# Performance work log

Measured on AMD Instinct MI355X. Metric: run time of the kernel, lower is better.

## Reference

```python
import jax, jax.numpy as jnp
import numpy as np

C = 128
NUM_GROUPS = 32  # min(32, 128 // 4)
EPS = 1e-6


def group_norm(x, gamma, beta):
    N, Cc, H, W = x.shape
    xg = x.reshape(N, NUM_GROUPS, -1)
    mean = xg.mean(axis=-1, keepdims=True)
    var = ((xg - mean) ** 2).mean(axis=-1, keepdims=True)
    xn = ((xg - mean) * jax.lax.rsqrt(var + EPS)).reshape(N, Cc, H, W)
    return xn * gamma[None, :, None, None] + beta[None, :, None, None]


def conv1x1(x, w, b):
    # w: [C_out, C_in], b: [C_out]; 1x1 conv == channel matmul
    return jnp.einsum('nchw,oc->nohw', x, w) + b[None, :, None, None]


def setup_inputs() -> dict:
    key = jax.random.key(0)
    ks = jax.random.split(key, 11)
    s = 1.0 / np.sqrt(C)
    return {
        'x': jax.random.normal(ks[0], (4, C, 64, 64), dtype=jnp.float32),
        'gamma': jnp.ones((C,), jnp.float32),
        'beta': jnp.zeros((C,), jnp.float32),
        'wq': jax.random.normal(ks[1], (C, C), jnp.float32) * s,
        'bq': jnp.zeros((C,), jnp.float32),
        'wk': jax.random.normal(ks[2], (C, C), jnp.float32) * s,
        'bk': jnp.zeros((C,), jnp.float32),
        'wv': jax.random.normal(ks[3], (C, C), jnp.float32) * s,
        'bv': jnp.zeros((C,), jnp.float32),
        'wo': jax.random.normal(ks[4], (C, C), jnp.float32) * s,
        'bo': jnp.zeros((C,), jnp.float32),
    }


def reference(x, gamma, beta, wq, bq, wk, bk, wv, bv, wo, bo):
    N, Cc, H, W = x.shape
    L = H * W
    xn = group_norm(x, gamma, beta)
    q = conv1x1(xn, wq, bq).reshape(N, Cc, L)  # [N,C,L]
    k = conv1x1(xn, wk, bk).reshape(N, Cc, L)
    v = conv1x1(xn, wv, bv).reshape(N, Cc, L)
    scale = 1.0 / jnp.sqrt(jnp.asarray(Cc, x.dtype))
    scores = jnp.einsum('ncl,ncm->nlm', q, k) * scale  # [N,L,L]
    weights = jax.nn.softmax(scores, axis=-1)
    attn = jnp.einsum('nlm,ncm->ncl', weights, v).reshape(N, Cc, H, W)
    return x + conv1x1(attn, wo, bo)
```

## Files before the change

### kernel.cpp

```cpp
#include <hip/hip_runtime.h>
#include <hip/hip_bf16.h>


#define N_B 4
#define C_D 128
#define L_D 4096
#define SPLIT 4
#define KVB 64
#define FSTEPS ((L_D/SPLIT)/KVB)
#define QSCALE (0.08838834764831845f * 1.4426950408889634f)
#define FIXM 16.0f

using f32x4  = __attribute__((ext_vector_type(4))) float;
using f32x16 = __attribute__((ext_vector_type(16))) float;
using bf16x8 = __attribute__((ext_vector_type(8))) short;

static __device__ __forceinline__ unsigned short f2bf(float f){
  return (unsigned short)((__builtin_bit_cast(unsigned int, f) + 0x8000u) >> 16);
}
static __device__ __forceinline__ float bf2f(unsigned short u){
  unsigned int x = ((unsigned int)u) << 16;
  return __builtin_bit_cast(float, x);
}
static __device__ __forceinline__ unsigned int pk2(float a, float b){
  unsigned int ua = __builtin_bit_cast(unsigned int, a) + 0x8000u;
  unsigned int ub = __builtin_bit_cast(unsigned int, b) + 0x8000u;
  return __builtin_amdgcn_perm(ub, ua, 0x07060302u);
}
static __device__ __forceinline__ float exp2a(float x){
  float r; asm("v_exp_f32 %0, %1" : "=v"(r) : "v"(x)); return r;
}
static __device__ __forceinline__ void gll16(const void* g, void* l){
  __builtin_amdgcn_global_load_lds(
      (const __attribute__((address_space(1))) unsigned int*)g,
      (__attribute__((address_space(3))) unsigned int*)l, 16, 0, 0);
}

__global__ __launch_bounds__(256) void gnw_k(
    const float* __restrict__ x, float* __restrict__ stats,
    const float* __restrict__ wq, const float* __restrict__ wk,
    const float* __restrict__ wv, const float* __restrict__ wo,
    unsigned short* __restrict__ wbf)
{
  int b = blockIdx.x, t = threadIdx.x;
  if (b >= 128){
    int b2 = b - 128;
    int mat = b2 >> 4;
    const float* src = (mat == 0) ? wq : (mat == 1) ? wk : (mat == 2) ? wv : wo;
    int off = (b2 & 15) * 1024 + t * 4;
    float4 v = *(const float4*)(src + off);
    *(uint2*)(wbf + mat*16384 + off) = make_uint2(pk2(v.x, v.y), pk2(v.z, v.w));
    return;
  }
  const float4* p = (const float4*)(x + (size_t)b * (4 * L_D));
  float s = 0.f, ss = 0.f;
#pragma unroll
  for (int i = 0; i < 16; ++i){
    float4 v = p[t + i*256];
    s  += v.x + v.y + v.z + v.w;
    ss += v.x*v.x + v.y*v.y + v.z*v.z + v.w*v.w;
  }
#pragma unroll
  for (int off = 32; off > 0; off >>= 1){
    s  += __shfl_down(s, off);
    ss += __shfl_down(ss, off);
  }
  __shared__ float rs4[4], rss4[4];
  if ((t & 63) == 0){ rs4[t>>6] = s; rss4[t>>6] = ss; }
  __syncthreads();
  if (t == 0){
    s  = rs4[0]+rs4[1]+rs4[2]+rs4[3];
    ss = rss4[0]+rss4[1]+rss4[2]+rss4[3];
    float mean = s * (1.f/16384.f);
    float var  = ss * (1.f/16384.f) - mean*mean;
    if (var < 0.f) var = 0.f;
    stats[2*b]   = mean;
    stats[2*b+1] = rsqrtf(var + 1e-6f);
  }
}

__global__ __launch_bounds__(256) void qkv_k(
    const float* __restrict__ x, const float* __restrict__ stats,
    const float* __restrict__ gamma, const float* __restrict__ beta,
    const unsigned short* __restrict__ wbf,
    const float* __restrict__ bq, const float* __restrict__ bk,
    const float* __restrict__ bv,
    unsigned short* __restrict__ q_ws, unsigned short* __restrict__ k_ws,
    unsigned short* __restrict__ v_ws)
{
  __shared__ unsigned short xnT[64][136];
  __shared__ unsigned short qbuf[64][136];

  int t = threadIdx.x, b = blockIdx.x;
  int wi = b >> 8;
  int bt = b & 255;
  int n = bt >> 6, l0 = (bt & 63) * 64;

  {
    int l = t & 63, cq = t >> 6;
#pragma unroll
    for (int it = 0; it < 8; ++it){
      int c0 = cq*4 + it*16;
      int g  = c0 >> 2;
      float mean = stats[(n*32+g)*2];
      float rstd = stats[(n*32+g)*2+1];
      float vv[4];
#pragma unroll
      for (int jj = 0; jj < 4; ++jj){
        int c = c0 + jj;
        float sc = rstd * gamma[c];
        float bs = beta[c] - mean * sc;
        vv[jj] = x[(size_t)(n*C_D + c)*L_D + l0 + l]*sc + bs;
      }
      *(unsigned int*)&xnT[l][c0]   = pk2(vv[0], vv[1]);
      *(unsigned int*)&xnT[l][c0+2] = pk2(vv[2], vv[3]);
    }
  }
  __syncthreads();

  int w = t >> 6, lane = t & 63, u = lane >> 4, l15 = lane & 15;
  int wc = w >> 1, wl = w & 1;
  const unsigned short* W = wbf + wi*16384;
  const float* Bv = (wi == 0) ? bq : (wi == 1) ? bk : bv;

  f32x4 zz = {0.f,0.f,0.f,0.f};
  f32x4 acc[4][2];
#pragma unroll
  for (int ct = 0; ct < 4; ++ct)
#pragma unroll
    for (int lt = 0; lt < 2; ++lt) acc[ct][lt] = zz;

#pragma unroll
  for (int kst = 0; kst < 4; ++kst){
    bf16x8 bfrag[2];
#pragma unroll
    for (int lt = 0; lt < 2; ++lt)
      bfrag[lt] = *(const bf16x8*)&xnT[32*wl + 16*lt + l15][kst*32 + 8*u];
#pragma unroll
    for (int ct = 0; ct < 4; ++ct){
      bf16x8 af = *(const bf16x8*)(W + (size_t)(64*wc + 16*ct + l15)*C_D + kst*32 + 8*u);
#pragma unroll
      for (int lt = 0; lt < 2; ++lt)
        acc[ct][lt] = __builtin_amdgcn_mfma_f32_16x16x32_bf16(af, bfrag[lt], acc[ct][lt], 0, 0, 0);
    }
  }

  if (wi < 2){
    float qs = (wi == 0) ? QSCALE : 1.0f;
#pragma unroll
    for (int ct = 0; ct < 4; ++ct){
      float bias[4];
#pragma unroll
      for (int r = 0; r < 4; ++r) bias[r] = Bv[64*wc + 16*ct + 4*u + r];
#pragma unroll
      for (int lt = 0; lt < 2; ++lt){
        float v0 = (acc[ct][lt][0] + bias[0]) * qs;
        float v1 = (acc[ct][lt][1] + bias[1]) * qs;
        float v2 = (acc[ct][lt][2] + bias[2]) * qs;
        float v3 = (acc[ct][lt][3] + bias[3]) * qs;
        int row = 32*wl + 16*lt + l15;
        int col = 64*wc + 16*ct + 4*u;
        *(unsigned int*)&qbuf[row][col]   = pk2(v0, v1);
        *(unsigned int*)&qbuf[row][col+2] = pk2(v2, v3);
      }
    }
    __syncthreads();
    {
      int l = t >> 2, ch = t & 3;
      unsigned short* dst = ((wi == 0) ? q_ws : k_ws) + (size_t)(n*L_D + l0 + l)*C_D + ch*32;
#pragma unroll
      for (int i = 0; i < 4; ++i)
        *(uint4*)(dst + i*8) = *(const uint4*)&qbuf[l][ch*32 + i*8];
    }
  } else {
    int p16 = (l15 & 3) | ((l15 & 4) << 1) | ((l15 & 8) >> 1);
#pragma unroll
    for (int ct = 0; ct < 4; ++ct){
      float bias[4];
#pragma unroll
      for (int r = 0; r < 4; ++r) bias[r] = Bv[64*wc + 16*ct + 4*u + r];
#pragma unroll
      for (int lt = 0; lt < 2; ++lt)
#pragma unroll
        for (int r = 0; r < 4; ++r){
          int co = 64*wc + 16*ct + 4*u + r;
          v_ws[(size_t)(n*C_D + co)*L_D + l0 + 32*wl + 16*lt + p16] =
              f2bf(acc[ct][lt][r] + bias[r]);
        }
    }
  }
}

__global__ __launch_bounds__(512, 2) void flash_split_k(
    const unsigned short* __restrict__ q_ws, const unsigned short* __restrict__ k_ws,
    const unsigned short* __restrict__ v_ws,
    unsigned short* __restrict__ po_ws, float* __restrict__ md_ws)
{
  __shared__ __align__(16) char shmem[131072];

  int t = threadIdx.x;
  int phys = blockIdx.x;
  int xcd = phys & 7, j = phys >> 3;
  int pair = xcd*8 + (j & 7);
  int s = j >> 3;
  int n = pair >> 4, lt256 = pair & 15;
  int l0 = lt256 * 256;
  int m_base = s * (L_D / SPLIT);
  int w = t >> 6, lane = t & 63, hi = lane >> 5, l31 = lane & 31;
  int lr = lane >> 4, ls = lane & 15;

  bf16x8 qf[8];
  {
    const unsigned short* qrow = q_ws + ((size_t)(n*L_D + l0 + 32*w + l31))*C_D;
#pragma unroll
    for (int kst = 0; kst < 8; ++kst)
      qf[kst] = *(const bf16x8*)(qrow + 16*kst + 8*hi);
  }

  f32x16 zz16;
#pragma unroll
  for (int i = 0; i < 16; ++i) zz16[i] = 0.f;
  f32x16 accO[4];
#pragma unroll
  for (int ct = 0; ct < 4; ++ct) accO[ct] = zz16;
  float rsum = 0.f;

  const unsigned short* kg[2];
  const unsigned short* vg[2];
  int ldof[2];
#pragma unroll
  for (int i = 0; i < 2; ++i){
    int row = 8*w + 4*i + lr;
    int ub = (ls << 4) ^ ((row & 15) << 4);
    kg[i] = k_ws + ((size_t)(n*L_D + m_base + row))*C_D + (ub >> 1);
    int c    = row + ((ub >> 7) << 6);
    int mloc = (ub & 127) >> 1;
    vg[i] = v_ws + ((size_t)(n*C_D + c))*L_D + m_base + mloc;
    ldof[i] = (8*w + 4*i)*256;
  }

#pragma unroll
  for (int pre = 0; pre < 3; ++pre){
    char* kD = shmem + (pre << 14);
    char* vD = shmem + 65536 + (pre << 14);
    gll16(kg[0] + (size_t)pre*KVB*C_D, kD + ldof[0]);
    gll16(kg[1] + (size_t)pre*KVB*C_D, kD + ldof[1]);
    gll16(vg[0] + pre*KVB, vD + ldof[0]);
    gll16(vg[1] + pre*KVB, vD + ldof[1]);
  }
  asm volatile("s_waitcnt vmcnt(8)" ::: "memory");
  __builtin_amdgcn_s_barrier();
  asm volatile("" ::: "memory");

#pragma unroll 4
  for (int step = 0; step < FSTEPS; ++step){
    int pf = step + 3; if (pf >= FSTEPS) pf = FSTEPS - 1;
    int pb = (step + 3) & 3;
    {
      char* kN = shmem + (pb << 14);
      char* vN = shmem + 65536 + (pb << 14);
      gll16(kg[0] + (size_t)pf*KVB*C_D, kN + ldof[0]);
      gll16(kg[1] + (size_t)pf*KVB*C_D, kN + ldof[1]);
      gll16(vg[0] + pf*KVB, vN + ldof[0]);
      gll16(vg[1] + pf*KVB, vN + ldof[1]);
    }

    char* kB = shmem + ((step & 3) << 14);
    char* vB = shmem + 65536 + ((step & 3) << 14);

    f32x16 accS[2];
#pragma unroll
    for (int mt = 0; mt < 2; ++mt) accS[mt] = zz16;
    __builtin_amdgcn_s_setprio(1);
#pragma unroll
    for (int mt = 0; mt < 2; ++mt){
      int row = 32*mt + l31;
      bf16x8 afr[8];
#pragma unroll
      for (int kst = 0; kst < 8; ++kst)
        afr[kst] = *(const bf16x8*)(kB + row*256 + ((32*kst + 16*hi) ^ ((row & 15) << 4)));
#pragma unroll
      for (int kst = 0; kst < 8; ++kst)
        accS[mt] = __builtin_amdgcn_mfma_f32_32x32x16_bf16(afr[kst], qf[kst], accS[mt], 0, 0, 0);
    }
    __builtin_amdgcn_s_setprio(0);

    union { unsigned int u[8]; bf16x8 h[2]; } Wm[2];
#pragma unroll
    for (int mt = 0; mt < 2; ++mt){
      float p[16];
#pragma unroll
      for (int r = 0; r < 16; ++r) p[r] = exp2a(accS[mt][r] - FIXM);
      float s0 = (p[0]+p[1])+(p[2]+p[3]),   s1 = (p[4]+p[5])+(p[6]+p[7]);
      float s2 = (p[8]+p[9])+(p[10]+p[11]), s3 = (p[12]+p[13])+(p[14]+p[15]);
      rsum += (s0+s1)+(s2+s3);
#pragma unroll
      for (int wd = 0; wd < 8; ++wd) Wm[mt].u[wd] = pk2(p[2*wd], p[2*wd+1]);
    }

    __builtin_amdgcn_s_setprio(1);
#pragma unroll
    for (int sl = 0; sl < 4; ++sl){
      bf16x8 pf2 = Wm[sl >> 1].h[sl & 1];
      bf16x8 vfr[4];
#pragma unroll
      for (int ct = 0; ct < 4; ++ct){
        int c = 32*ct + l31, vrow = c & 63;
        int lb = ((c >> 6) << 7) + 32*sl + 16*hi;
        vfr[ct] = *(const bf16x8*)(vB + vrow*256 + (lb ^ ((vrow & 15) << 4)));
      }
#pragma unroll
      for (int ct = 0; ct < 4; ++ct)
        accO[ct] = __builtin_amdgcn_mfma_f32_32x32x16_bf16(vfr[ct], pf2, accO[ct], 0, 0, 0);
    }
    __builtin_amdgcn_s_setprio(0);

    asm volatile("s_waitcnt vmcnt(8)" ::: "memory");
    __builtin_amdgcn_s_barrier();
    asm volatile("" ::: "memory");
  }

  asm volatile("s_waitcnt vmcnt(0)" ::: "memory");
  __builtin_amdgcn_s_barrier();
  asm volatile("" ::: "memory");

  rsum += __shfl_xor(rsum, 32);

  char* tB = shmem;
  {
    int lloc = 32*w + l31;
    int tsw = (lloc & 15) << 4;
    char* tr = tB + (size_t)lloc*256;
#pragma unroll
    for (int ct = 0; ct < 4; ++ct)
#pragma unroll
      for (int q = 0; q < 4; ++q){
        int cb2 = 64*ct + 16*q + 8*hi;
        *(unsigned int*)(tr + ((cb2    ) ^ tsw)) = pk2(accO[ct][4*q+0], accO[ct][4*q+1]);
        *(unsigned int*)(tr + ((cb2 + 4) ^ tsw)) = pk2(accO[ct][4*q+2], accO[ct][4*q+3]);
      }
  }
  __syncthreads();
  {
    int row2 = t >> 1, hf2 = t & 1;
    int tile = row2 >> 7, lrow = row2 & 127;
    size_t pb = ((size_t)((n*32 + 2*lt256 + tile)*SPLIT + s)) * (size_t)(128*128);
    unsigned short* dst = po_ws + pb + (size_t)lrow*128 + hf2*64;
    const char* srcr = tB + row2*256;
    int sw2 = (row2 & 15) << 4;
#pragma unroll
    for (int i = 0; i < 8; ++i)
      *(uint4*)(dst + 8*i) = *(const uint4*)(srcr + ((hf2*128 + 16*i) ^ sw2));
  }
  if (lane < 32){
    int lg = 32*w + lane;
    int tile2 = lg >> 7, lrow2 = lg & 127;
    size_t mb2 = ((size_t)((n*32 + 2*lt256 + tile2)*SPLIT + s)) * 128;
    md_ws[mb2 + lrow2] = rsum;
  }
}

__global__ __launch_bounds__(256) void combine_k(
    const unsigned short* __restrict__ po_ws, const float* __restrict__ md_ws,
    const float* __restrict__ x, const unsigned short* __restrict__ wo_bf,
    const float* __restrict__ bo, float* __restrict__ out)
{
  __shared__ __align__(16) char aB[16384];

  int t = threadIdx.x, b = blockIdx.x;
  int xcd = b & 7, j = b >> 3;
  int pair = xcd*8 + (j & 7);
  int quarter = j >> 3;
  int n = pair >> 4, lt256 = pair & 15;
  int lt64 = lt256*4 + quarter;
  int f = lt64 >> 1, loff = (lt64 & 1)*64, l0 = lt64*64;
  size_t pbase = ((size_t)((n*32 + f)*SPLIT)) * (size_t)(128*128);
  size_t mbase = ((size_t)((n*32 + f)*SPLIT)) * 128;

  {
    int l = t >> 2, q = t & 3;
    float Dg = 0.f;
#pragma unroll
    for (int s2 = 0; s2 < SPLIT; ++s2)
      Dg += md_ws[mbase + s2*128 + loff + l];
    float inv = 1.0f / Dg;

    float a[32];
#pragma unroll
    for (int i = 0; i < 32; ++i) a[i] = 0.f;
#pragma unroll
    for (int s2 = 0; s2 < SPLIT; ++s2){
      const uint4* p = (const uint4*)(po_ws + pbase + (size_t)s2*(128*128)
                                      + (size_t)(loff + l)*128 + q*32);
#pragma unroll
      for (int i = 0; i < 4; ++i){
        uint4 uv = p[i];
        unsigned int uu[4] = {uv.x, uv.y, uv.z, uv.w};
#pragma unroll
        for (int j2 = 0; j2 < 4; ++j2){
          a[8*i + 2*j2]     += bf2f((unsigned short)(uu[j2] & 0xffffu));
          a[8*i + 2*j2 + 1] += bf2f((unsigned short)(uu[j2] >> 16));
        }
      }
    }
    char* ar = aB + l*256;
    int asw = (l & 7) << 4;
#pragma unroll
    for (int i = 0; i < 16; ++i){
      int cb = q*64 + 4*i;
      *(unsigned int*)(ar + (cb ^ asw)) = pk2(a[2*i]*inv, a[2*i+1]*inv);
    }
  }
  __syncthreads();

  int w = t >> 6, lane = t & 63, hi = lane >> 5, l31 = lane & 31;
  int lh = w >> 1, ch = w & 1;
  f32x16 acc[2];
#pragma unroll
  for (int ci = 0; ci < 2; ++ci)
#pragma unroll
    for (int i = 0; i < 16; ++i) acc[ci][i] = 0.f;

#pragma unroll
  for (int kst = 0; kst < 8; ++kst){
    int row = 32*lh + l31;
    bf16x8 bfg = *(const bf16x8*)(aB + row*256 + ((32*kst + 16*hi) ^ ((row & 7) << 4)));
#pragma unroll
    for (int ci = 0; ci < 2; ++ci){
      bf16x8 af = *(const bf16x8*)(wo_bf + (size_t)(64*ch + 32*ci + l31)*C_D + 16*kst + 8*hi);
      acc[ci] = __builtin_amdgcn_mfma_f32_32x32x16_bf16(af, bfg, acc[ci], 0, 0, 0);
    }
  }
#pragma unroll
  for (int ci = 0; ci < 2; ++ci)
#pragma unroll
    for (int r = 0; r < 16; ++r){
      int o = 64*ch + 32*ci + (r & 3) + 8*(r >> 2) + 4*hi;
      size_t idx = (size_t)(n*C_D + o)*L_D + l0 + 32*lh + l31;
      out[idx] = x[idx] + bo[o] + acc[ci][r];
    }
}

extern "C" void kernel_launch(void* const* d_in, const int* in_sizes, int n_in,
                              void* d_out, int out_size, void* d_ws, size_t ws_size,
                              hipStream_t stream) {
  const float* x     = (const float*)d_in[0];
  const float* gamma = (const float*)d_in[1];
  const float* beta  = (const float*)d_in[2];
  const float* wq    = (const float*)d_in[3];
  const float* bq    = (const float*)d_in[4];
  const float* wk    = (const float*)d_in[5];
  const float* bk    = (const float*)d_in[6];
  const float* wv    = (const float*)d_in[7];
  const float* bv    = (const float*)d_in[8];
  const float* wo    = (const float*)d_in[9];
  const float* bo    = (const float*)d_in[10];
  float* out = (float*)d_out;

  char* ws = (char*)d_ws;
  float* stats          = (float*)ws;
  unsigned short* q_ws  = (unsigned short*)(ws + 4096);
  unsigned short* k_ws  = q_ws + (size_t)N_B * L_D * C_D;
  unsigned short* v_ws  = k_ws + (size_t)N_B * L_D * C_D;
  unsigned short* po_ws = v_ws + (size_t)N_B * L_D * C_D;
  float* md_ws          = (float*)(po_ws + (size_t)N_B * 32 * SPLIT * 128 * 128);
  unsigned short* wbf   = (unsigned short*)(md_ws + (size_t)N_B * 32 * SPLIT * 128);

  gnw_k<<<192, 256, 0, stream>>>(x, stats, wq, wk, wv, wo, wbf);
  qkv_k<<<768, 256, 0, stream>>>(x, stats, gamma, beta, wbf, bq, bk, bv,
                                 q_ws, k_ws, v_ws);
  flash_split_k<<<256, 512, 0, stream>>>(q_ws, k_ws, v_ws, po_ws, md_ws);
  combine_k<<<256, 256, 0, stream>>>(po_ws, md_ws, x, wbf + 3*16384, bo, out);
}
```

Before: 73.52 us.

## Software-pipeline flash loop so QK of next tile overlaps softmax and PV

Restructures the split-K flash attention main loop into a software pipeline. The QK^T scores for the next KV tile are computed while exp2/pack of the previous scores and the PV MFMAs on the previous V tile run interleaved in the same step. The loop is manually unrolled by two with ping-pong score registers. Prefetch distance drops from 3 to 2 tiles to free an LDS buffer for the lagging V tile. This aims to hide transcendental and packing latency behind matrix-core work, at the cost of more live registers and a shallower global prefetch.

```diff
diff --git a/kernel.cpp b/kernel.cpp
--- a/kernel.cpp
+++ b/kernel.cpp
@@ -191,6 +191,105 @@
   }
 }
 
+#define STEPBODY(STEP, SIN0, SIN1, SOUT0, SOUT1, DOQK)                           \
+  {                                                                              \
+    const int step_ = (STEP);                                                    \
+    int pfi = step_ + 2; if (pfi > FSTEPS-1) pfi = FSTEPS-1;                     \
+    int pbb = (step_ + 2) & 3;                                                   \
+    {                                                                            \
+      char* kN = shmem + (pbb << 14);                                            \
+      char* vN = shmem + 65536 + (pbb << 14);                                    \
+      gll16(kg[0] + (size_t)pfi*KVB*C_D, kN + ldof[0]);                          \
+      gll16(kg[1] + (size_t)pfi*KVB*C_D, kN + ldof[1]);                          \
+      gll16(vg[0] + pfi*KVB, vN + ldof[0]);                                      \
+      gll16(vg[1] + pfi*KVB, vN + ldof[1]);                                      \
+    }                                                                            \
+    char* kB = shmem + ((step_ & 3) << 14);                                      \
+    char* vP = shmem + 65536 + (((step_ - 1) & 3) << 14);                        \
+    const bool doQK = (DOQK);                                                    \
+    float p0[16], p1[16];                                                        \
+    union Wu { unsigned int u[8]; bf16x8 h[2]; } Wm0, Wm1;                       \
+    __builtin_amdgcn_s_setprio(1);                                               \
+                                  \
+    if (doQK){                                                                   \
+      bf16x8 afr[8];                                                             \
+      _Pragma("unroll")                                                          \
+      for (int k = 0; k < 8; ++k)                                                \
+        afr[k] = *(const bf16x8*)(kB + l31*256 +                                 \
+                   ((32*k + 16*hi) ^ ((l31 & 15) << 4)));                        \
+      SOUT0 = zz16;                                                              \
+      _Pragma("unroll")                                                          \
+      for (int k = 0; k < 8; ++k){                                               \
+        SOUT0 = __builtin_amdgcn_mfma_f32_32x32x16_bf16(afr[k], qf[k], SOUT0, 0, 0, 0); \
+        p0[2*k]   = exp2a(SIN0[2*k]   - FIXM);                                   \
+        p0[2*k+1] = exp2a(SIN0[2*k+1] - FIXM);                                   \
+      }                                                                          \
+    } else {                                                                     \
+      _Pragma("unroll")                                                          \
+      for (int r = 0; r < 16; ++r) p0[r] = exp2a(SIN0[r] - FIXM);                \
+    }                                                                            \
+                                     \
+    if (doQK){                                                                   \
+      bf16x8 afr[8];                                                             \
+      _Pragma("unroll")                                                          \
+      for (int k = 0; k < 8; ++k)                                                \
+        afr[k] = *(const bf16x8*)(kB + (32 + l31)*256 +                          \
+                   ((32*k + 16*hi) ^ ((l31 & 15) << 4)));                        \
+      SOUT1 = zz16;                                                              \
+      _Pragma("unroll")                                                          \
+      for (int k = 0; k < 8; ++k){                                               \
+        SOUT1 = __builtin_amdgcn_mfma_f32_32x32x16_bf16(afr[k], qf[k], SOUT1, 0, 0, 0); \
+        Wm0.u[k] = pk2(p0[2*k], p0[2*k+1]);                                      \
+      }                                                                          \
+    } else {                                                                     \
+      _Pragma("unroll")                                                          \
+      for (int k = 0; k < 8; ++k) Wm0.u[k] = pk2(p0[2*k], p0[2*k+1]);            \
+    }                                                                            \
+    rsum += (((p0[0]+p0[1])+(p0[2]+p0[3])) + ((p0[4]+p0[5])+(p0[6]+p0[7])))      \
+          + (((p0[8]+p0[9])+(p0[10]+p0[11])) + ((p0[12]+p0[13])+(p0[14]+p0[15])));\
+                                \
+    _Pragma("unroll")                                                            \
+    for (int sl = 0; sl < 2; ++sl){                                              \
+      bf16x8 pfv = Wm0.h[sl];                                                    \
+      bf16x8 vfr[4];                                                             \
+      _Pragma("unroll")                                                          \
+      for (int ct = 0; ct < 4; ++ct){                                            \
+        int c = 32*ct + l31, vrow = c & 63;                                      \
+        int lb = ((c >> 6) << 7) + 32*sl + 16*hi;                                \
+        vfr[ct] = *(const bf16x8*)(vP + vrow*256 + (lb ^ ((vrow & 15) << 4)));   \
+      }                                                                          \
+      _Pragma("unroll")                                                          \
+      for (int ct = 0; ct < 4; ++ct){                                            \
+        accO[ct] = __builtin_amdgcn_mfma_f32_32x32x16_bf16(vfr[ct], pfv, accO[ct], 0, 0, 0); \
+        p1[8*sl + 2*ct]     = exp2a(SIN1[8*sl + 2*ct]     - FIXM);               \
+        p1[8*sl + 2*ct + 1] = exp2a(SIN1[8*sl + 2*ct + 1] - FIXM);               \
+      }                                                                          \
+    }                                                                            \
+    _Pragma("unroll")                                                            \
+    for (int k = 0; k < 8; ++k) Wm1.u[k] = pk2(p1[2*k], p1[2*k+1]);              \
+    rsum += (((p1[0]+p1[1])+(p1[2]+p1[3])) + ((p1[4]+p1[5])+(p1[6]+p1[7])))      \
+          + (((p1[8]+p1[9])+(p1[10]+p1[11])) + ((p1[12]+p1[13])+(p1[14]+p1[15])));\
+                                                            \
+    _Pragma("unroll")                                                            \
+    for (int sl = 2; sl < 4; ++sl){                                              \
+      bf16x8 pfv = Wm1.h[sl & 1];                                                \
+      bf16x8 vfr[4];                                                             \
+      _Pragma("unroll")                                                          \
+      for (int ct = 0; ct < 4; ++ct){                                            \
+        int c = 32*ct + l31, vrow = c & 63;                                      \
+        int lb = ((c >> 6) << 7) + 32*sl + 16*hi;                                \
+        vfr[ct] = *(const bf16x8*)(vP + vrow*256 + (lb ^ ((vrow & 15) << 4)));   \
+      }                                                                          \
+      _Pragma("unroll")                                                          \
+      for (int ct = 0; ct < 4; ++ct)                                             \
+        accO[ct] = __builtin_amdgcn_mfma_f32_32x32x16_bf16(vfr[ct], pfv, accO[ct], 0, 0, 0); \
+    }                                                                            \
+    __builtin_amdgcn_s_setprio(0);                                               \
+    asm volatile("s_waitcnt vmcnt(4)" ::: "memory");                             \
+    __builtin_amdgcn_s_barrier();                                                \
+    asm volatile("" ::: "memory");                                               \
+  }
+
 __global__ __launch_bounds__(512, 2) void flash_split_k(
     const unsigned short* __restrict__ q_ws, const unsigned short* __restrict__ k_ws,
     const unsigned short* __restrict__ v_ws,
@@ -248,76 +347,33 @@
     gll16(vg[0] + pre*KVB, vD + ldof[0]);
     gll16(vg[1] + pre*KVB, vD + ldof[1]);
   }
-  asm volatile("s_waitcnt vmcnt(8)" ::: "memory");
+  asm volatile("s_waitcnt vmcnt(4)" ::: "memory");
   __builtin_amdgcn_s_barrier();
   asm volatile("" ::: "memory");
 
-#pragma unroll 4
-  for (int step = 0; step < FSTEPS; ++step){
-    int pf = step + 3; if (pf >= FSTEPS) pf = FSTEPS - 1;
-    int pb = (step + 3) & 3;
-    {
-      char* kN = shmem + (pb << 14);
-      char* vN = shmem + 65536 + (pb << 14);
-      gll16(kg[0] + (size_t)pf*KVB*C_D, kN + ldof[0]);
-      gll16(kg[1] + (size_t)pf*KVB*C_D, kN + ldof[1]);
-      gll16(vg[0] + pf*KVB, vN + ldof[0]);
-      gll16(vg[1] + pf*KVB, vN + ldof[1]);
-    }
-
-    char* kB = shmem + ((step & 3) << 14);
-    char* vB = shmem + 65536 + ((step & 3) << 14);
-
-    f32x16 accS[2];
-#pragma unroll
-    for (int mt = 0; mt < 2; ++mt) accS[mt] = zz16;
+  f32x16 sA0, sA1, sB0, sB1;
+  {
     __builtin_amdgcn_s_setprio(1);
-#pragma unroll
-    for (int mt = 0; mt < 2; ++mt){
-      int row = 32*mt + l31;
-      bf16x8 afr[8];
-#pragma unroll
-      for (int kst = 0; kst < 8; ++kst)
-        afr[kst] = *(const bf16x8*)(kB + row*256 + ((32*kst + 16*hi) ^ ((row & 15) << 4)));
-#pragma unroll
-      for (int kst = 0; kst < 8; ++kst)
-        accS[mt] = __builtin_amdgcn_mfma_f32_32x32x16_bf16(afr[kst], qf[kst], accS[mt], 0, 0, 0);
-    }
+    sA0 = zz16; sA1 = zz16;
+    bf16x8 afr[8];
+#pragma unroll
+    for (int k = 0; k < 8; ++k)
+      afr[k] = *(const bf16x8*)(shmem + l31*256 + ((32*k + 16*hi) ^ ((l31 & 15) << 4)));
+#pragma unroll
+    for (int k = 0; k < 8; ++k)
+      sA0 = __builtin_amdgcn_mfma_f32_32x32x16_bf16(afr[k], qf[k], sA0, 0, 0, 0);
+#pragma unroll
+    for (int k = 0; k < 8; ++k)
+      afr[k] = *(const bf16x8*)(shmem + (32 + l31)*256 + ((32*k + 16*hi) ^ ((l31 & 15) << 4)));
+#pragma unroll
+    for (int k = 0; k < 8; ++k)
+      sA1 = __builtin_amdgcn_mfma_f32_32x32x16_bf16(afr[k], qf[k], sA1, 0, 0, 0);
     __builtin_amdgcn_s_setprio(0);
-
-    union { unsigned int u[8]; bf16x8 h[2]; } Wm[2];
-#pragma unroll
-    for (int mt = 0; mt < 2; ++mt){
-      float p[16];
-#pragma unroll
-      for (int r = 0; r < 16; ++r) p[r] = exp2a(accS[mt][r] - FIXM);
-      float s0 = (p[0]+p[1])+(p[2]+p[3]),   s1 = (p[4]+p[5])+(p[6]+p[7]);
-      float s2 = (p[8]+p[9])+(p[10]+p[11]), s3 = (p[12]+p[13])+(p[14]+p[15]);
-      rsum += (s0+s1)+(s2+s3);
-#pragma unroll
-      for (int wd = 0; wd < 8; ++wd) Wm[mt].u[wd] = pk2(p[2*wd], p[2*wd+1]);
-    }
-
-    __builtin_amdgcn_s_setprio(1);
-#pragma unroll
-    for (int sl = 0; sl < 4; ++sl){
-      bf16x8 pf2 = Wm[sl >> 1].h[sl & 1];
-      bf16x8 vfr[4];
-#pragma unroll
-      for (int ct = 0; ct < 4; ++ct){
-        int c = 32*ct + l31, vrow = c & 63;
-        int lb = ((c >> 6) << 7) + 32*sl + 16*hi;
-        vfr[ct] = *(const bf16x8*)(vB + vrow*256 + (lb ^ ((vrow & 15) << 4)));
-      }
-#pragma unroll
-      for (int ct = 0; ct < 4; ++ct)
-        accO[ct] = __builtin_amdgcn_mfma_f32_32x32x16_bf16(vfr[ct], pf2, accO[ct], 0, 0, 0);
-    }
-    __builtin_amdgcn_s_setprio(0);
-
-    asm volatile("s_waitcnt vmcnt(8)" ::: "memory");
-    __builtin_amdgcn_s_barrier();
-    asm volatile("" ::: "memory");
+  }
+
+  for (int e = 1; e < 17; e += 2){
+    STEPBODY(e,     sA0, sA1, sB0, sB1, true)
+    STEPBODY(e + 1, sB0, sB1, sA0, sA1, (e + 1 < FSTEPS))
   }
 
   asm volatile("s_waitcnt vmcnt(0)" ::: "memory");
```

New measurement: 73.74 us. About the same (+0.3%).

## Software-pipeline flash loop so QK of next tile overlaps softmax and PV

Applied to the files above, without the earlier changes.

Restructures the split-K flash attention main loop into a software pipeline. Each phase computes QK scores for tile u while exp2 and PV for tile u-1 are interleaved with the MFMAs, using ping-pong score registers. Prefetch depth drops from three tiles ahead to two, and extra barriers split each step into four sub-phases so that waves stay in lockstep. The aim is to hide exp/pack latency behind matrix ops, at the cost of more barriers, higher register pressure and a shallower prefetch.

```diff
diff --git a/kernel.cpp b/kernel.cpp
--- a/kernel.cpp
+++ b/kernel.cpp
@@ -191,6 +191,122 @@
   }
 }
 
+#define BARRIER() do { __builtin_amdgcn_s_barrier(); asm volatile("" ::: "memory"); } while(0)
+
+#define PHASESTEP(U, SIN0, SIN1, SOUT0, SOUT1, DOQK, DOPV)                       \
+  {                                                                              \
+    const int u_ = (U);                                                          \
+    char* kB = shmem + ((u_ & 3) << 14);                                         \
+    char* vP = shmem + 65536 + (((u_ - 1) & 3) << 14);                           \
+    const bool doQK = (DOQK), doPV = (DOPV);                                     \
+    float p0[16], p1[16];                                                        \
+    union Wu { unsigned int u[8]; bf16x8 h[2]; } Wm0, Wm1;                       \
+             \
+    {                                                                            \
+      bf16x8 afr[8];                                                             \
+      if (doQK){                                                                 \
+        _Pragma("unroll")                                                        \
+        for (int k = 0; k < 8; ++k)                                              \
+          afr[k] = *(const bf16x8*)(kB + l31*256 + ((32*k + 16*hi) ^ swz));      \
+      }                                                                          \
+      { int nu = u_ + 2; int nk = nu > FSTEPS-1 ? FSTEPS-1 : nu;                 \
+        char* kN = shmem + ((nu & 3) << 14);                                     \
+        char* vN = shmem + 65536 + ((nu & 3) << 14);                             \
+        gll16(kg[0] + (size_t)nk*KVB*C_D, kN + ldof[0]);                         \
+        gll16(kg[1] + (size_t)nk*KVB*C_D, kN + ldof[1]);                         \
+        gll16(vg[0] + nk*KVB, vN + ldof[0]);                                     \
+        gll16(vg[1] + nk*KVB, vN + ldof[1]); }                                   \
+      BARRIER();                                                                 \
+      __builtin_amdgcn_s_setprio(1);                                             \
+      if (doQK) SOUT0 = zz16;                                                    \
+      _Pragma("unroll")                                                          \
+      for (int k = 0; k < 8; ++k){                                               \
+        if (doQK) SOUT0 = __builtin_amdgcn_mfma_f32_32x32x16_bf16(afr[k], qf[k], SOUT0, 0, 0, 0); \
+        if (doPV){ p0[2*k] = exp2a(SIN0[2*k] - FIXM);                            \
+                   p0[2*k+1] = exp2a(SIN0[2*k+1] - FIXM); }                      \
+      }                                                                          \
+      __builtin_amdgcn_s_setprio(0);                                             \
+      BARRIER();                                                                 \
+    }                                                                            \
+                        \
+    {                                                                            \
+      bf16x8 afr[8];                                                             \
+      if (doQK){                                                                 \
+        _Pragma("unroll")                                                        \
+        for (int k = 0; k < 8; ++k)                                              \
+          afr[k] = *(const bf16x8*)(kB + (32 + l31)*256 + ((32*k + 16*hi) ^ swz)); \
+      }                                                                          \
+      BARRIER();                                                                 \
+      __builtin_amdgcn_s_setprio(1);                                             \
+      if (doQK) SOUT1 = zz16;                                                    \
+      _Pragma("unroll")                                                          \
+      for (int k = 0; k < 8; ++k){                                               \
+        if (doQK) SOUT1 = __builtin_amdgcn_mfma_f32_32x32x16_bf16(afr[k], qf[k], SOUT1, 0, 0, 0); \
+        if (doPV) Wm0.u[k] = pk2(p0[2*k], p0[2*k+1]);                            \
+      }                                                                          \
+      if (doPV)                                                                  \
+        rsum += (((p0[0]+p0[1])+(p0[2]+p0[3])) + ((p0[4]+p0[5])+(p0[6]+p0[7])))  \
+              + (((p0[8]+p0[9])+(p0[10]+p0[11])) + ((p0[12]+p0[13])+(p0[14]+p0[15]))); \
+      __builtin_amdgcn_s_setprio(0);                                             \
+      BARRIER();                                                                 \
+    }                                                                            \
+    if (doPV){                                                                   \
+                   \
+      {                                                                          \
+        bf16x8 vfr[8];                                                           \
+        _Pragma("unroll")                                                        \
+        for (int sl = 0; sl < 2; ++sl)                                           \
+        _Pragma("unroll")                                                        \
+        for (int ct = 0; ct < 4; ++ct){                                          \
+          int c = 32*ct + l31, vrow = c & 63;                                    \
+          int lb = ((c >> 6) << 7) + 32*sl + 16*hi;                              \
+          vfr[4*sl+ct] = *(const bf16x8*)(vP + vrow*256 + (lb ^ swz));           \
+        }                                                                        \
+        BARRIER();                                                               \
+        __builtin_amdgcn_s_setprio(1);                                           \
+        _Pragma("unroll")                                                        \
+        for (int sl = 0; sl < 2; ++sl)                                           \
+        _Pragma("unroll")                                                        \
+        for (int ct = 0; ct < 4; ++ct){                                          \
+          accO[ct] = __builtin_amdgcn_mfma_f32_32x32x16_bf16(vfr[4*sl+ct], Wm0.h[sl], accO[ct], 0, 0, 0); \
+          p1[8*sl + 2*ct]     = exp2a(SIN1[8*sl + 2*ct]     - FIXM);             \
+          p1[8*sl + 2*ct + 1] = exp2a(SIN1[8*sl + 2*ct + 1] - FIXM);             \
+        }                                                                        \
+        __builtin_amdgcn_s_setprio(0);                                           \
+        BARRIER();                                                               \
+      }                                                                          \
+       \
+      {                                                                          \
+        bf16x8 vfr[8];                                                           \
+        _Pragma("unroll")                                                        \
+        for (int sl = 0; sl < 2; ++sl)                                           \
+        _Pragma("unroll")                                                        \
+        for (int ct = 0; ct < 4; ++ct){                                          \
+          int c = 32*ct + l31, vrow = c & 63;                                    \
+          int lb = ((c >> 6) << 7) + 32*(sl+2) + 16*hi;                          \
+          vfr[4*sl+ct] = *(const bf16x8*)(vP + vrow*256 + (lb ^ swz));           \
+        }                                                                        \
+        BARRIER();                                                               \
+        __builtin_amdgcn_s_setprio(1);                                           \
+        _Pragma("unroll")                                                        \
+        for (int k = 0; k < 8; ++k) Wm1.u[k] = pk2(p1[2*k], p1[2*k+1]);          \
+        _Pragma("unroll")                                                        \
+        for (int sl = 0; sl < 2; ++sl)                                           \
+        _Pragma("unroll")                                                        \
+        for (int ct = 0; ct < 4; ++ct)                                           \
+          accO[ct] = __builtin_amdgcn_mfma_f32_32x32x16_bf16(vfr[4*sl+ct], Wm1.h[sl], accO[ct], 0, 0, 0); \
+        rsum += (((p1[0]+p1[1])+(p1[2]+p1[3])) + ((p1[4]+p1[5])+(p1[6]+p1[7])))  \
+              + (((p1[8]+p1[9])+(p1[10]+p1[11])) + ((p1[12]+p1[13])+(p1[14]+p1[15]))); \
+        __builtin_amdgcn_s_setprio(0);                                           \
+        asm volatile("s_waitcnt vmcnt(4)" ::: "memory");                         \
+        BARRIER();                                                               \
+      }                                                                          \
+    } else {                                                                     \
+      asm volatile("s_waitcnt vmcnt(4)" ::: "memory");                           \
+      BARRIER();                                                                 \
+    }                                                                            \
+  }
+
 __global__ __launch_bounds__(512, 2) void flash_split_k(
     const unsigned short* __restrict__ q_ws, const unsigned short* __restrict__ k_ws,
     const unsigned short* __restrict__ v_ws,
@@ -208,6 +324,7 @@
   int m_base = s * (L_D / SPLIT);
   int w = t >> 6, lane = t & 63, hi = lane >> 5, l31 = lane & 31;
   int lr = lane >> 4, ls = lane & 15;
+  int swz = (l31 & 15) << 4;
 
   bf16x8 qf[8];
   {
@@ -239,90 +356,29 @@
     ldof[i] = (8*w + 4*i)*256;
   }
 
-#pragma unroll
-  for (int pre = 0; pre < 3; ++pre){
-    char* kD = shmem + (pre << 14);
-    char* vD = shmem + 65536 + (pre << 14);
-    gll16(kg[0] + (size_t)pre*KVB*C_D, kD + ldof[0]);
-    gll16(kg[1] + (size_t)pre*KVB*C_D, kD + ldof[1]);
-    gll16(vg[0] + pre*KVB, vD + ldof[0]);
-    gll16(vg[1] + pre*KVB, vD + ldof[1]);
-  }
-  asm volatile("s_waitcnt vmcnt(8)" ::: "memory");
-  __builtin_amdgcn_s_barrier();
-  asm volatile("" ::: "memory");
-
-#pragma unroll 4
-  for (int step = 0; step < FSTEPS; ++step){
-    int pf = step + 3; if (pf >= FSTEPS) pf = FSTEPS - 1;
-    int pb = (step + 3) & 3;
-    {
-      char* kN = shmem + (pb << 14);
-      char* vN = shmem + 65536 + (pb << 14);
-      gll16(kg[0] + (size_t)pf*KVB*C_D, kN + ldof[0]);
-      gll16(kg[1] + (size_t)pf*KVB*C_D, kN + ldof[1]);
-      gll16(vg[0] + pf*KVB, vN + ldof[0]);
-      gll16(vg[1] + pf*KVB, vN + ldof[1]);
-    }
-
-    char* kB = shmem + ((step & 3) << 14);
-    char* vB = shmem + 65536 + ((step & 3) << 14);
-
-    f32x16 accS[2];
-#pragma unroll
-    for (int mt = 0; mt < 2; ++mt) accS[mt] = zz16;
-    __builtin_amdgcn_s_setprio(1);
-#pragma unroll
-    for (int mt = 0; mt < 2; ++mt){
-      int row = 32*mt + l31;
-      bf16x8 afr[8];
-#pragma unroll
-      for (int kst = 0; kst < 8; ++kst)
-        afr[kst] = *(const bf16x8*)(kB + row*256 + ((32*kst + 16*hi) ^ ((row & 15) << 4)));
-#pragma unroll
-      for (int kst = 0; kst < 8; ++kst)
-        accS[mt] = __builtin_amdgcn_mfma_f32_32x32x16_bf16(afr[kst], qf[kst], accS[mt], 0, 0, 0);
-    }
-    __builtin_amdgcn_s_setprio(0);
-
-    union { unsigned int u[8]; bf16x8 h[2]; } Wm[2];
-#pragma unroll
-    for (int mt = 0; mt < 2; ++mt){
-      float p[16];
-#pragma unroll
-      for (int r = 0; r < 16; ++r) p[r] = exp2a(accS[mt][r] - FIXM);
-      float s0 = (p[0]+p[1])+(p[2]+p[3]),   s1 = (p[4]+p[5])+(p[6]+p[7]);
-      float s2 = (p[8]+p[9])+(p[10]+p[11]), s3 = (p[12]+p[13])+(p[14]+p[15]);
-      rsum += (s0+s1)+(s2+s3);
-#pragma unroll
-      for (int wd = 0; wd < 8; ++wd) Wm[mt].u[wd] = pk2(p[2*wd], p[2*wd+1]);
-    }
-
-    __builtin_amdgcn_s_setprio(1);
-#pragma unroll
-    for (int sl = 0; sl < 4; ++sl){
-      bf16x8 pf2 = Wm[sl >> 1].h[sl & 1];
-      bf16x8 vfr[4];
-#pragma unroll
-      for (int ct = 0; ct < 4; ++ct){
-        int c = 32*ct + l31, vrow = c & 63;
-        int lb = ((c >> 6) << 7) + 32*sl + 16*hi;
-        vfr[ct] = *(const bf16x8*)(vB + vrow*256 + (lb ^ ((vrow & 15) << 4)));
-      }
-#pragma unroll
-      for (int ct = 0; ct < 4; ++ct)
-        accO[ct] = __builtin_amdgcn_mfma_f32_32x32x16_bf16(vfr[ct], pf2, accO[ct], 0, 0, 0);
-    }
-    __builtin_amdgcn_s_setprio(0);
-
-    asm volatile("s_waitcnt vmcnt(8)" ::: "memory");
-    __builtin_amdgcn_s_barrier();
-    asm volatile("" ::: "memory");
-  }
+  gll16(kg[0], shmem + ldof[0]);
+  gll16(kg[1], shmem + ldof[1]);
+  gll16(vg[0], shmem + 65536 + ldof[0]);
+  gll16(vg[1], shmem + 65536 + ldof[1]);
+  gll16(kg[0] + (size_t)KVB*C_D, shmem + 16384 + ldof[0]);
+  gll16(kg[1] + (size_t)KVB*C_D, shmem + 16384 + ldof[1]);
+  gll16(vg[0] + KVB, shmem + 65536 + 16384 + ldof[0]);
+  gll16(vg[1] + KVB, shmem + 65536 + 16384 + ldof[1]);
+  asm volatile("s_waitcnt vmcnt(4)" ::: "memory");
+  BARRIER();
+
+  f32x16 sA0, sA1, sB0 = zz16, sB1 = zz16;
+
+  PHASESTEP(0, sB0, sB1, sA0, sA1, true, false)
+  for (int e = 1; e < 15; e += 2){
+    PHASESTEP(e,     sA0, sA1, sB0, sB1, true, true)
+    PHASESTEP(e + 1, sB0, sB1, sA0, sA1, true, true)
+  }
+  PHASESTEP(15, sA0, sA1, sB0, sB1, true,  true)
+  PHASESTEP(16, sB0, sB1, sA0, sA1, false, true)
 
   asm volatile("s_waitcnt vmcnt(0)" ::: "memory");
-  __builtin_amdgcn_s_barrier();
-  asm volatile("" ::: "memory");
+  BARRIER();
 
   rsum += __shfl_xor(rsum, 32);
 
```

New measurement: 74.87 us. About the same (+1.8%).

## Software-pipeline QK^T one step ahead of softmax/PV with wave-parity ping-pong

Applied to the files above, without the earlier changes.

Restructures the flash-attention main loop so the QK^T scores for step i+1 are computed in the same iteration as the softmax and PV for step i, using double-buffered score registers. Odd and even waves run the phases in opposite order, so MFMA work from one wave overlaps exp/pack VALU work from another. Prefetch depth drops from 3 to 2 tiles ahead and the wait counts are adjusted to match. The aim is to hide the softmax VALU latency behind matrix work. In exchange it raises register pressure under the 512-thread launch bound and leaves less time for global loads to arrive.

```diff
diff --git a/kernel.cpp b/kernel.cpp
--- a/kernel.cpp
+++ b/kernel.cpp
@@ -191,6 +191,95 @@
   }
 }
 
+
+#define QKPART(SOUT0, SOUT1)                                                \
+  {                                                                         \
+    bf16x8 afr[8];                                                          \
+    _Pragma("unroll")                                                       \
+    for (int k = 0; k < 8; ++k)                                             \
+      afr[k] = *(const bf16x8*)(kB + l31*256 + ((32*k + 16*hi) ^ swz));     \
+    SOUT0 = zz16;                                                           \
+    __builtin_amdgcn_s_setprio(1);                                          \
+    _Pragma("unroll")                                                       \
+    for (int k = 0; k < 8; ++k)                                             \
+      SOUT0 = __builtin_amdgcn_mfma_f32_32x32x16_bf16(afr[k], qf[k], SOUT0, 0, 0, 0); \
+    __builtin_amdgcn_s_setprio(0);                                          \
+    _Pragma("unroll")                                                       \
+    for (int k = 0; k < 8; ++k)                                             \
+      afr[k] = *(const bf16x8*)(kB + (32 + l31)*256 + ((32*k + 16*hi) ^ swz)); \
+    SOUT1 = zz16;                                                           \
+    __builtin_amdgcn_s_setprio(1);                                          \
+    _Pragma("unroll")                                                       \
+    for (int k = 0; k < 8; ++k)                                             \
+      SOUT1 = __builtin_amdgcn_mfma_f32_32x32x16_bf16(afr[k], qf[k], SOUT1, 0, 0, 0); \
+    __builtin_amdgcn_s_setprio(0);                                          \
+  }
+
+#define SMPART(SIN0, SIN1)                                                  \
+  {                                                                         \
+    float p[16];                                                            \
+    _Pragma("unroll")                                                       \
+    for (int r = 0; r < 16; ++r) p[r] = exp2a(SIN0[r] - FIXM);              \
+    _Pragma("unroll")                                                       \
+    for (int k = 0; k < 8; ++k) Wm0.u[k] = pk2(p[2*k], p[2*k+1]);           \
+    rsum += (((p[0]+p[1])+(p[2]+p[3])) + ((p[4]+p[5])+(p[6]+p[7])))         \
+          + (((p[8]+p[9])+(p[10]+p[11])) + ((p[12]+p[13])+(p[14]+p[15])));  \
+    _Pragma("unroll")                                                       \
+    for (int r = 0; r < 16; ++r) p[r] = exp2a(SIN1[r] - FIXM);              \
+    _Pragma("unroll")                                                       \
+    for (int k = 0; k < 8; ++k) Wm1.u[k] = pk2(p[2*k], p[2*k+1]);           \
+    rsum += (((p[0]+p[1])+(p[2]+p[3])) + ((p[4]+p[5])+(p[6]+p[7])))         \
+          + (((p[8]+p[9])+(p[10]+p[11])) + ((p[12]+p[13])+(p[14]+p[15])));  \
+  }
+
+#define PVPART()                                                            \
+  _Pragma("unroll")                                                         \
+  for (int sl = 0; sl < 4; ++sl){                                           \
+    bf16x8 pfv = (sl < 2) ? Wm0.h[sl] : Wm1.h[sl & 1];                      \
+    bf16x8 vfr[4];                                                          \
+    _Pragma("unroll")                                                       \
+    for (int ct = 0; ct < 4; ++ct){                                         \
+      int c = 32*ct + l31, vrow = c & 63;                                   \
+      int lb = ((c >> 6) << 7) + 32*sl + 16*hi;                             \
+      vfr[ct] = *(const bf16x8*)(vP + vrow*256 + (lb ^ ((vrow & 15) << 4)));\
+    }                                                                       \
+    __builtin_amdgcn_s_setprio(1);                                          \
+    _Pragma("unroll")                                                       \
+    for (int ct = 0; ct < 4; ++ct)                                          \
+      accO[ct] = __builtin_amdgcn_mfma_f32_32x32x16_bf16(vfr[ct], pfv, accO[ct], 0, 0, 0); \
+    __builtin_amdgcn_s_setprio(0);                                          \
+  }
+
+#define STEPBODY(STEP, SIN0, SIN1, SOUT0, SOUT1, DOQK)                      \
+  {                                                                         \
+    const int step_ = (STEP);                                               \
+    int pfi = step_ + 2; if (pfi > FSTEPS-1) pfi = FSTEPS-1;                \
+    int pbb = (step_ + 2) & 3;                                              \
+    {                                                                       \
+      char* kN = shmem + (pbb << 14);                                       \
+      char* vN = shmem + 65536 + (pbb << 14);                               \
+      gll16(kg[0] + (size_t)pfi*KVB*C_D, kN + ldof[0]);                     \
+      gll16(kg[1] + (size_t)pfi*KVB*C_D, kN + ldof[1]);                     \
+      gll16(vg[0] + pfi*KVB, vN + ldof[0]);                                 \
+      gll16(vg[1] + pfi*KVB, vN + ldof[1]);                                 \
+    }                                                                       \
+    char* kB = shmem + ((step_ & 3) << 14);                                 \
+    char* vP = shmem + 65536 + (((step_ - 1) & 3) << 14);                   \
+    union Wu { unsigned int u[8]; bf16x8 h[2]; } Wm0, Wm1;                  \
+    if (wodd){                                                              \
+      SMPART(SIN0, SIN1)                                                    \
+      PVPART()                                                              \
+      if (DOQK) QKPART(SOUT0, SOUT1)                                        \
+    } else {                                                                \
+      if (DOQK) QKPART(SOUT0, SOUT1)                                        \
+      SMPART(SIN0, SIN1)                                                    \
+      PVPART()                                                              \
+    }                                                                       \
+    asm volatile("s_waitcnt vmcnt(4)" ::: "memory");                        \
+    __builtin_amdgcn_s_barrier();                                           \
+    asm volatile("" ::: "memory");                                          \
+  }
+
 __global__ __launch_bounds__(512, 2) void flash_split_k(
     const unsigned short* __restrict__ q_ws, const unsigned short* __restrict__ k_ws,
     const unsigned short* __restrict__ v_ws,
@@ -208,6 +297,8 @@
   int m_base = s * (L_D / SPLIT);
   int w = t >> 6, lane = t & 63, hi = lane >> 5, l31 = lane & 31;
   int lr = lane >> 4, ls = lane & 15;
+  int swz = (l31 & 15) << 4;
+  const bool wodd = (w & 1);
 
   bf16x8 qf[8];
   {
@@ -248,76 +339,34 @@
     gll16(vg[0] + pre*KVB, vD + ldof[0]);
     gll16(vg[1] + pre*KVB, vD + ldof[1]);
   }
-  asm volatile("s_waitcnt vmcnt(8)" ::: "memory");
+  asm volatile("s_waitcnt vmcnt(4)" ::: "memory");
   __builtin_amdgcn_s_barrier();
   asm volatile("" ::: "memory");
 
-#pragma unroll 4
-  for (int step = 0; step < FSTEPS; ++step){
-    int pf = step + 3; if (pf >= FSTEPS) pf = FSTEPS - 1;
-    int pb = (step + 3) & 3;
-    {
-      char* kN = shmem + (pb << 14);
-      char* vN = shmem + 65536 + (pb << 14);
-      gll16(kg[0] + (size_t)pf*KVB*C_D, kN + ldof[0]);
-      gll16(kg[1] + (size_t)pf*KVB*C_D, kN + ldof[1]);
-      gll16(vg[0] + pf*KVB, vN + ldof[0]);
-      gll16(vg[1] + pf*KVB, vN + ldof[1]);
-    }
-
-    char* kB = shmem + ((step & 3) << 14);
-    char* vB = shmem + 65536 + ((step & 3) << 14);
-
-    f32x16 accS[2];
-#pragma unroll
-    for (int mt = 0; mt < 2; ++mt) accS[mt] = zz16;
+  f32x16 sA0, sA1, sB0, sB1;
+  {
+    char* kB = shmem;
     __builtin_amdgcn_s_setprio(1);
-#pragma unroll
-    for (int mt = 0; mt < 2; ++mt){
-      int row = 32*mt + l31;
-      bf16x8 afr[8];
-#pragma unroll
-      for (int kst = 0; kst < 8; ++kst)
-        afr[kst] = *(const bf16x8*)(kB + row*256 + ((32*kst + 16*hi) ^ ((row & 15) << 4)));
-#pragma unroll
-      for (int kst = 0; kst < 8; ++kst)
-        accS[mt] = __builtin_amdgcn_mfma_f32_32x32x16_bf16(afr[kst], qf[kst], accS[mt], 0, 0, 0);
-    }
+    sA0 = zz16; sA1 = zz16;
+    bf16x8 afr[8];
+#pragma unroll
+    for (int k = 0; k < 8; ++k)
+      afr[k] = *(const bf16x8*)(kB + l31*256 + ((32*k + 16*hi) ^ swz));
+#pragma unroll
+    for (int k = 0; k < 8; ++k)
+      sA0 = __builtin_amdgcn_mfma_f32_32x32x16_bf16(afr[k], qf[k], sA0, 0, 0, 0);
+#pragma unroll
+    for (int k = 0; k < 8; ++k)
+      afr[k] = *(const bf16x8*)(kB + (32 + l31)*256 + ((32*k + 16*hi) ^ swz));
+#pragma unroll
+    for (int k = 0; k < 8; ++k)
+      sA1 = __builtin_amdgcn_mfma_f32_32x32x16_bf16(afr[k], qf[k], sA1, 0, 0, 0);
     __builtin_amdgcn_s_setprio(0);
-
-    union { unsigned int u[8]; bf16x8 h[2]; } Wm[2];
-#pragma unroll
-    for (int mt = 0; mt < 2; ++mt){
-      float p[16];
-#pragma unroll
-      for (int r = 0; r < 16; ++r) p[r] = exp2a(accS[mt][r] - FIXM);
-      float s0 = (p[0]+p[1])+(p[2]+p[3]),   s1 = (p[4]+p[5])+(p[6]+p[7]);
-      float s2 = (p[8]+p[9])+(p[10]+p[11]), s3 = (p[12]+p[13])+(p[14]+p[15]);
-      rsum += (s0+s1)+(s2+s3);
-#pragma unroll
-      for (int wd = 0; wd < 8; ++wd) Wm[mt].u[wd] = pk2(p[2*wd], p[2*wd+1]);
-    }
-
-    __builtin_amdgcn_s_setprio(1);
-#pragma unroll
-    for (int sl = 0; sl < 4; ++sl){
-      bf16x8 pf2 = Wm[sl >> 1].h[sl & 1];
-      bf16x8 vfr[4];
-#pragma unroll
-      for (int ct = 0; ct < 4; ++ct){
-        int c = 32*ct + l31, vrow = c & 63;
-        int lb = ((c >> 6) << 7) + 32*sl + 16*hi;
-        vfr[ct] = *(const bf16x8*)(vB + vrow*256 + (lb ^ ((vrow & 15) << 4)));
-      }
-#pragma unroll
-      for (int ct = 0; ct < 4; ++ct)
-        accO[ct] = __builtin_amdgcn_mfma_f32_32x32x16_bf16(vfr[ct], pf2, accO[ct], 0, 0, 0);
-    }
-    __builtin_amdgcn_s_setprio(0);
-
-    asm volatile("s_waitcnt vmcnt(8)" ::: "memory");
-    __builtin_amdgcn_s_barrier();
-    asm volatile("" ::: "memory");
+  }
+
+  for (int e = 1; e < 17; e += 2){
+    STEPBODY(e,     sA0, sA1, sB0, sB1, true)
+    STEPBODY(e + 1, sB0, sB1, sA0, sA1, (e + 2 < FSTEPS))
   }
 
   asm volatile("s_waitcnt vmcnt(0)" ::: "memory");
```

New measurement: 76.06 us. 1.03x slower.
